# Performance work log

Measured on AMD Instinct MI355X. Metric: run time of the kernel, lower is better.

## Reference

```python
import jax, jax.numpy as jnp
import numpy as np

EPS = 1e-10
R, H, W = 8192, 1024, 1024


def setup_inputs() -> dict:
    key = jax.random.key(0)
    k1, k2, k3, k4, k5, k6 = jax.random.split(key, 6)
    seg = jax.random.normal(k1, (1, 2, H, W), dtype=jnp.float32)
    score = jax.random.uniform(k2, (R, 1), dtype=jnp.float32)
    # boxes with guaranteed non-empty regions (x2>x1, y2>y1)
    x1 = jax.random.randint(k3, (R,), 0, W - 1)
    y1 = jax.random.randint(k4, (R,), 0, H - 1)
    w = jax.random.randint(k5, (R,), 1, W)
    h = jax.random.randint(k6, (R,), 1, H)
    x2 = jnp.minimum(x1 + w, W)
    y2 = jnp.minimum(y1 + h, H)
    ssw = jnp.stack([jnp.zeros_like(x1), x1, y1, x2, y2], axis=1)[None].astype(jnp.int32)
    return {"ssw": ssw, "seg": seg, "score": score}


def reference(ssw, seg, score):
    boxes = ssw[0, :, 1:]                      # [R,4] = x1,y1,x2,y2
    seg = jax.nn.softmax(seg, axis=1)
    score_map = seg[0, 1]                      # [H,W]
    # Summed-area table: region mean for every ROI in one vectorized pass
    # (replaces the per-ROI python-loop slicing in the original).
    P = jnp.pad(jnp.cumsum(jnp.cumsum(score_map, axis=0), axis=1), ((1, 0), (1, 0)))
    x1, y1, x2, y2 = boxes[:, 0], boxes[:, 1], boxes[:, 2], boxes[:, 3]
    sums = P[y2, x2] - P[y1, x2] - P[y2, x1] + P[y1, x1]
    area = ((y2 - y1) * (x2 - x1)).astype(score_map.dtype)
    iou = sums / area                          # [R] per-ROI mean score
    # pairwise smooth-abs differences
    sim_iou = jnp.sqrt((iou[:, None] - iou[None, :]) ** 2 + EPS)     # [R,R]
    s = score.reshape(-1)
    sim_score = jnp.sqrt((s[:, None] - s[None, :]) ** 2 + EPS)        # [R,R]
    return jnp.mean((sim_iou - sim_score) ** 2)
```

## Files before the change

### kernel.cpp

```cpp
#include <hip/hip_runtime.h>
#include <math.h>

#define HH 1024
#define WW 1024
#define RR 8192
#define EPSD 1e-10

#define OFF_C     4194304
#define OFF_BSUM  12582912
#define OFF_IOU   13107200
#define OFF_STAT  13139968

__device__ __forceinline__ float sigm(float a, float b) {
    float z = (a - b) * 1.44269504088896f;
    float e = __builtin_amdgcn_exp2f(z);
    return __builtin_amdgcn_rcpf(1.0f + e);
}

__global__ void row_scan(const float* __restrict__ seg, float* __restrict__ rowpref,
                         double* __restrict__ stats) {
    if (blockIdx.x == 0 && threadIdx.x < 5) stats[threadIdx.x] = 0.0;
    const int h = blockIdx.x;
    const int t = threadIdx.x;
    const float4* s0 = (const float4*)(seg + (size_t)h * WW);
    const float4* s1 = (const float4*)(seg + (size_t)(HH * WW) + (size_t)h * WW);
    float4 a = s0[t];
    float4 b = s1[t];
    float p0 = sigm(a.x, b.x);
    float p1 = p0 + sigm(a.y, b.y);
    float p2 = p1 + sigm(a.z, b.z);
    float p3 = p2 + sigm(a.w, b.w);

    float tsum = p3;
    const int lane = t & 63, wid = t >> 6;
    #pragma unroll
    for (int off = 1; off < 64; off <<= 1) {
        float n = __shfl_up(tsum, off, 64);
        if (lane >= off) tsum += n;
    }
    __shared__ float wsum[4];
    if (lane == 63) wsum[wid] = tsum;
    __syncthreads();
    float woff = 0.0f;
    for (int k = 0; k < wid; ++k) woff += wsum[k];
    const float excl = woff + tsum - p3;

    float4 o;
    o.x = excl + p0;
    o.y = excl + p1;
    o.z = excl + p2;
    o.w = excl + p3;
    ((float4*)(rowpref + (size_t)h * WW))[t] = o;
}

__global__ void col_partial(const float* __restrict__ rowpref, double* __restrict__ bsum) {
    const int w = blockIdx.x * 256 + threadIdx.x;
    const int chunk = blockIdx.y;
    const int r0 = chunk * 16;
    double acc = 0.0;
    #pragma unroll
    for (int r = r0; r < r0 + 16; ++r) acc += (double)rowpref[(size_t)r * WW + w];
    bsum[chunk * WW + w] = acc;
}

__global__ void col_scan(const float* __restrict__ rowpref, const double* __restrict__ bsum,
                         double* __restrict__ C) {
    const int w = blockIdx.x * 256 + threadIdx.x;
    const int chunk = blockIdx.y;
    double acc = 0.0;
    for (int k = 0; k < chunk; ++k) acc += bsum[k * WW + w];
    const int r0 = chunk * 16;
    #pragma unroll
    for (int r = r0; r < r0 + 16; ++r) {
        acc += (double)rowpref[(size_t)r * WW + w];
        C[(size_t)r * WW + w] = acc;
    }
}

__global__ void box_stats(const int* __restrict__ ssw, const double* __restrict__ C,
                          const float* __restrict__ score,
                          float* __restrict__ iou, double* __restrict__ stats) {
    const int r = blockIdx.x * 256 + threadIdx.x;
    const int* b = ssw + r * 5;
    const int x1 = b[1], y1 = b[2], x2 = b[3], y2 = b[4];
    double p22 = C[(size_t)(y2 - 1) * WW + (x2 - 1)];
    double p12 = (y1 > 0) ? C[(size_t)(y1 - 1) * WW + (x2 - 1)] : 0.0;
    double p21 = (x1 > 0) ? C[(size_t)(y2 - 1) * WW + (x1 - 1)] : 0.0;
    double p11 = (y1 > 0 && x1 > 0) ? C[(size_t)(y1 - 1) * WW + (x1 - 1)] : 0.0;
    double sums = p22 - p12 - p21 + p11;
    double area = (double)((y2 - y1) * (x2 - x1));
    double u = sums / area;
    iou[r] = (float)u;
    double s = (double)score[r];

    double v0 = u, v1 = u * u, v2 = s, v3 = s * s;
    #pragma unroll
    for (int off = 32; off; off >>= 1) {
        v0 += __shfl_down(v0, off, 64);
        v1 += __shfl_down(v1, off, 64);
        v2 += __shfl_down(v2, off, 64);
        v3 += __shfl_down(v3, off, 64);
    }
    if ((threadIdx.x & 63) == 0) {
        atomicAdd(&stats[0], v0);
        atomicAdd(&stats[1], v1);
        atomicAdd(&stats[2], v2);
        atomicAdd(&stats[3], v3);
    }
}

#define KI 4
#define JT 128
__global__ void pair_prod(const float* __restrict__ iou, const float* __restrict__ score,
                          double* __restrict__ stats) {
    __shared__ float ju[JT];
    __shared__ float js[JT];
    const int t = threadIdx.x;
    const int j0 = blockIdx.y * JT;
    if (t < JT) ju[t] = iou[j0 + t];
    else js[t - JT] = score[j0 + t - JT];

    const int i0 = blockIdx.x * (256 * KI) + t;
    float iu[KI], isc[KI];
    #pragma unroll
    for (int k = 0; k < KI; ++k) {
        iu[k]  = iou[i0 + 256 * k];
        isc[k] = score[i0 + 256 * k];
    }
    __syncthreads();

    float acc[KI];
    #pragma unroll
    for (int k = 0; k < KI; ++k) acc[k] = 0.0f;
    #pragma unroll 8
    for (int j = 0; j < JT; ++j) {
        const float uj = ju[j];
        const float sj = js[j];
        #pragma unroll
        for (int k = 0; k < KI; ++k) {
            float du = iu[k] - uj;
            float ds = isc[k] - sj;
            acc[k] += fabsf(du * ds);
        }
    }
    float afl = (acc[0] + acc[1]) + (acc[2] + acc[3]);
    double v = (double)afl;
    #pragma unroll
    for (int off = 32; off; off >>= 1) v += __shfl_down(v, off, 64);
    __shared__ double wred[4];
    const int lane = t & 63, wid = t >> 6;
    if (lane == 0) wred[wid] = v;
    __syncthreads();
    if (t == 0) atomicAdd(&stats[4], wred[0] + wred[1] + wred[2] + wred[3]);
}

__global__ void finalize(const double* __restrict__ stats, float* __restrict__ out) {
    const double R = (double)RR;
    double Su = stats[0], Su2 = stats[1], Ss = stats[2], Ss2 = stats[3], Sab = stats[4];
    double lossR2 = 2.0 * R * Su2 - 2.0 * Su * Su
                  + 2.0 * R * Ss2 - 2.0 * Ss * Ss
                  + 2.0 * R * R * EPSD
                  - 2.0 * Sab;
    out[0] = (float)(lossR2 / (R * R));
}

extern "C" void kernel_launch(void* const* d_in, const int* in_sizes, int n_in,
                              void* d_out, int out_size, void* d_ws, size_t ws_size,
                              hipStream_t stream) {
    const int*   ssw   = (const int*)d_in[0];
    const float* seg   = (const float*)d_in[1];
    const float* score = (const float*)d_in[2];

    float*  rowpref = (float*)d_ws;
    double* C       = (double*)((char*)d_ws + OFF_C);
    double* bsum    = (double*)((char*)d_ws + OFF_BSUM);
    float*  iou     = (float*)((char*)d_ws + OFF_IOU);
    double* stats   = (double*)((char*)d_ws + OFF_STAT);

    row_scan<<<HH, 256, 0, stream>>>(seg, rowpref, stats);
    col_partial<<<dim3(4, 64), 256, 0, stream>>>(rowpref, bsum);
    col_scan<<<dim3(4, 64), 256, 0, stream>>>(rowpref, bsum, C);
    box_stats<<<RR / 256, 256, 0, stream>>>(ssw, C, score, iou, stats);
    pair_prod<<<dim3(RR / (256 * KI), RR / JT), 256, 0, stream>>>(iou, score, stats);
    finalize<<<1, 1, 0, stream>>>(stats, (float*)d_out);
}
```

Before: 108.4 us.

## Fuse column scan passes via flag chaining and fold finalize into pair kernel

```diff
diff --git a/kernel.cpp b/kernel.cpp
--- a/kernel.cpp
+++ b/kernel.cpp
@@ -10,6 +10,10 @@
 #define OFF_BSUM  12582912
 #define OFF_IOU   13107200
 #define OFF_STAT  13139968
+#define OFF_FLAG  13140032
+#define OFF_TICK  13141056
+
+typedef float v2f __attribute__((ext_vector_type(2)));
 
 __device__ __forceinline__ float sigm(float a, float b) {
     float z = (a - b) * 1.44269504088896f;
@@ -17,9 +21,16 @@
     return __builtin_amdgcn_rcpf(1.0f + e);
 }
 
-__global__ void row_scan(const float* __restrict__ seg, float* __restrict__ rowpref,
-                         double* __restrict__ stats) {
-    if (blockIdx.x == 0 && threadIdx.x < 5) stats[threadIdx.x] = 0.0;
+__global__ __launch_bounds__(256) void row_scan(const float* __restrict__ seg,
+                                                float* __restrict__ rowpref,
+                                                double* __restrict__ stats,
+                                                unsigned* __restrict__ flags,
+                                                unsigned* __restrict__ ticket) {
+    if (blockIdx.x == 0) {
+        if (threadIdx.x < 5) stats[threadIdx.x] = 0.0;
+        flags[threadIdx.x] = 0u;
+        if (threadIdx.x == 0) *ticket = 0u;
+    }
     const int h = blockIdx.x;
     const int t = threadIdx.x;
     const float4* s0 = (const float4*)(seg + (size_t)h * WW);
@@ -53,34 +64,53 @@
     ((float4*)(rowpref + (size_t)h * WW))[t] = o;
 }
 
-__global__ void col_partial(const float* __restrict__ rowpref, double* __restrict__ bsum) {
-    const int w = blockIdx.x * 256 + threadIdx.x;
+__global__ __launch_bounds__(256) void col_scan_fused(const float* __restrict__ rowpref,
+                                                      double* __restrict__ bsum,
+                                                      double* __restrict__ C,
+                                                      unsigned* __restrict__ flags) {
+    const int c = blockIdx.x;
     const int chunk = blockIdx.y;
+    const int t = threadIdx.x;
+    const int w = c * 256 + t;
     const int r0 = chunk * 16;
+
+    double part[16];
     double acc = 0.0;
     #pragma unroll
-    for (int r = r0; r < r0 + 16; ++r) acc += (double)rowpref[(size_t)r * WW + w];
+    for (int r = 0; r < 16; ++r) {
+        acc += (double)rowpref[(size_t)(r0 + r) * WW + w];
+        part[r] = acc;
+    }
     bsum[chunk * WW + w] = acc;
-}
-
-__global__ void col_scan(const float* __restrict__ rowpref, const double* __restrict__ bsum,
-                         double* __restrict__ C) {
-    const int w = blockIdx.x * 256 + threadIdx.x;
-    const int chunk = blockIdx.y;
-    double acc = 0.0;
-    for (int k = 0; k < chunk; ++k) acc += bsum[k * WW + w];
-    const int r0 = chunk * 16;
-    #pragma unroll
-    for (int r = r0; r < r0 + 16; ++r) {
-        acc += (double)rowpref[(size_t)r * WW + w];
-        C[(size_t)r * WW + w] = acc;
-    }
-}
-
-__global__ void box_stats(const int* __restrict__ ssw, const double* __restrict__ C,
-                          const float* __restrict__ score,
-                          float* __restrict__ iou, double* __restrict__ stats) {
-    const int r = blockIdx.x * 256 + threadIdx.x;
+    __syncthreads();
+    __threadfence();
+    if (t == 0)
+        __hip_atomic_store(&flags[chunk * 4 + c], 1u,
+                           __ATOMIC_RELEASE, __HIP_MEMORY_SCOPE_AGENT);
+
+    if (t == 0) {
+        for (int kp = 0; kp < chunk; ++kp)
+            while (__hip_atomic_load(&flags[kp * 4 + c],
+                                     __ATOMIC_RELAXED, __HIP_MEMORY_SCOPE_AGENT) == 0u) {}
+    }
+    __syncthreads();
+    __threadfence();
+
+    double base = 0.0;
+    #pragma unroll 4
+    for (int kp = 0; kp < chunk; ++kp) base += bsum[kp * WW + w];
+
+    #pragma unroll
+    for (int r = 0; r < 16; ++r)
+        C[(size_t)(r0 + r) * WW + w] = base + part[r];
+}
+
+__global__ __launch_bounds__(128) void box_stats(const int* __restrict__ ssw,
+                                                 const double* __restrict__ C,
+                                                 const float* __restrict__ score,
+                                                 float* __restrict__ iou,
+                                                 double* __restrict__ stats) {
+    const int r = blockIdx.x * 128 + threadIdx.x;
     const int* b = ssw + r * 5;
     const int x1 = b[1], y1 = b[2], x2 = b[3], y2 = b[4];
     double p22 = C[(size_t)(y2 - 1) * WW + (x2 - 1)];
@@ -111,39 +141,47 @@
 
 #define KI 4
 #define JT 128
-__global__ void pair_prod(const float* __restrict__ iou, const float* __restrict__ score,
-                          double* __restrict__ stats) {
-    __shared__ float ju[JT];
-    __shared__ float js[JT];
+__global__ __launch_bounds__(256) void pair_prod(const float* __restrict__ iou,
+                                                 const float* __restrict__ score,
+                                                 double* __restrict__ stats,
+                                                 float* __restrict__ out,
+                                                 unsigned* __restrict__ ticket) {
+    __shared__ v2f ju[JT / 2];
+    __shared__ v2f js[JT / 2];
     const int t = threadIdx.x;
     const int j0 = blockIdx.y * JT;
-    if (t < JT) ju[t] = iou[j0 + t];
-    else js[t - JT] = score[j0 + t - JT];
+    if (t < JT / 2) ju[t] = ((const v2f*)(iou + j0))[t];
+    else if (t < JT) js[t - JT / 2] = ((const v2f*)(score + j0))[t - JT / 2];
 
     const int i0 = blockIdx.x * (256 * KI) + t;
-    float iu[KI], isc[KI];
+    v2f iuv[KI], isv[KI];
     #pragma unroll
     for (int k = 0; k < KI; ++k) {
-        iu[k]  = iou[i0 + 256 * k];
-        isc[k] = score[i0 + 256 * k];
-    }
-    __syncthreads();
-
-    float acc[KI];
-    #pragma unroll
-    for (int k = 0; k < KI; ++k) acc[k] = 0.0f;
-    #pragma unroll 8
-    for (int j = 0; j < JT; ++j) {
-        const float uj = ju[j];
-        const float sj = js[j];
+        float u = iou[i0 + 256 * k];
+        float s = score[i0 + 256 * k];
+        iuv[k] = (v2f){u, u};
+        isv[k] = (v2f){s, s};
+    }
+    __syncthreads();
+
+    float ax[KI], ay[KI];
+    #pragma unroll
+    for (int k = 0; k < KI; ++k) { ax[k] = 0.0f; ay[k] = 0.0f; }
+    #pragma unroll 4
+    for (int j = 0; j < JT / 2; ++j) {
+        const v2f uj = ju[j];
+        const v2f sj = js[j];
         #pragma unroll
         for (int k = 0; k < KI; ++k) {
-            float du = iu[k] - uj;
-            float ds = isc[k] - sj;
-            acc[k] += fabsf(du * ds);
+            v2f du = iuv[k] - uj;
+            v2f ds = isv[k] - sj;
+            v2f p  = du * ds;
+            ax[k] += fabsf(p.x);
+            ay[k] += fabsf(p.y);
         }
     }
-    float afl = (acc[0] + acc[1]) + (acc[2] + acc[3]);
+    float afl = ((ax[0] + ay[0]) + (ax[1] + ay[1]))
+              + ((ax[2] + ay[2]) + (ax[3] + ay[3]));
     double v = (double)afl;
     #pragma unroll
     for (int off = 32; off; off >>= 1) v += __shfl_down(v, off, 64);
@@ -151,17 +189,25 @@
     const int lane = t & 63, wid = t >> 6;
     if (lane == 0) wred[wid] = v;
     __syncthreads();
-    if (t == 0) atomicAdd(&stats[4], wred[0] + wred[1] + wred[2] + wred[3]);
-}
-
-__global__ void finalize(const double* __restrict__ stats, float* __restrict__ out) {
-    const double R = (double)RR;
-    double Su = stats[0], Su2 = stats[1], Ss = stats[2], Ss2 = stats[3], Sab = stats[4];
-    double lossR2 = 2.0 * R * Su2 - 2.0 * Su * Su
-                  + 2.0 * R * Ss2 - 2.0 * Ss * Ss
-                  + 2.0 * R * R * EPSD
-                  - 2.0 * Sab;
-    out[0] = (float)(lossR2 / (R * R));
+    if (t == 0) {
+        atomicAdd(&stats[4], wred[0] + wred[1] + wred[2] + wred[3]);
+        __threadfence();
+        unsigned tk = atomicAdd(ticket, 1u);
+        if (tk == (unsigned)(gridDim.x * gridDim.y - 1)) {
+            __threadfence();
+            double Su  = __hip_atomic_load(&stats[0], __ATOMIC_RELAXED, __HIP_MEMORY_SCOPE_AGENT);
+            double Su2 = __hip_atomic_load(&stats[1], __ATOMIC_RELAXED, __HIP_MEMORY_SCOPE_AGENT);
+            double Ss  = __hip_atomic_load(&stats[2], __ATOMIC_RELAXED, __HIP_MEMORY_SCOPE_AGENT);
+            double Ss2 = __hip_atomic_load(&stats[3], __ATOMIC_RELAXED, __HIP_MEMORY_SCOPE_AGENT);
+            double Sab = __hip_atomic_load(&stats[4], __ATOMIC_RELAXED, __HIP_MEMORY_SCOPE_AGENT);
+            const double R = (double)RR;
+            double lossR2 = 2.0 * R * Su2 - 2.0 * Su * Su
+                          + 2.0 * R * Ss2 - 2.0 * Ss * Ss
+                          + 2.0 * R * R * EPSD
+                          - 2.0 * Sab;
+            out[0] = (float)(lossR2 / (R * R));
+        }
+    }
 }
 
 extern "C" void kernel_launch(void* const* d_in, const int* in_sizes, int n_in,
@@ -171,16 +217,16 @@
     const float* seg   = (const float*)d_in[1];
     const float* score = (const float*)d_in[2];
 
-    float*  rowpref = (float*)d_ws;
-    double* C       = (double*)((char*)d_ws + OFF_C);
-    double* bsum    = (double*)((char*)d_ws + OFF_BSUM);
-    float*  iou     = (float*)((char*)d_ws + OFF_IOU);
-    double* stats   = (double*)((char*)d_ws + OFF_STAT);
-
-    row_scan<<<HH, 256, 0, stream>>>(seg, rowpref, stats);
-    col_partial<<<dim3(4, 64), 256, 0, stream>>>(rowpref, bsum);
-    col_scan<<<dim3(4, 64), 256, 0, stream>>>(rowpref, bsum, C);
-    box_stats<<<RR / 256, 256, 0, stream>>>(ssw, C, score, iou, stats);
-    pair_prod<<<dim3(RR / (256 * KI), RR / JT), 256, 0, stream>>>(iou, score, stats);
-    finalize<<<1, 1, 0, stream>>>(stats, (float*)d_out);
-}
+    float*    rowpref = (float*)d_ws;
+    double*   C       = (double*)((char*)d_ws + OFF_C);
+    double*   bsum    = (double*)((char*)d_ws + OFF_BSUM);
+    float*    iou     = (float*)((char*)d_ws + OFF_IOU);
+    double*   stats   = (double*)((char*)d_ws + OFF_STAT);
+    unsigned* flags   = (unsigned*)((char*)d_ws + OFF_FLAG);
+    unsigned* ticket  = (unsigned*)((char*)d_ws + OFF_TICK);
+
+    row_scan<<<HH, 256, 0, stream>>>(seg, rowpref, stats, flags, ticket);
+    col_scan_fused<<<dim3(4, 64), 256, 0, stream>>>(rowpref, bsum, C, flags);
+    box_stats<<<RR / 128, 128, 0, stream>>>(ssw, C, score, iou, stats);
+    pair_prod<<<dim3(RR / (256 * KI), RR / JT), 256, 0, stream>>>(iou, score, stats, (float*)d_out, ticket);
+}
```

Result: slower. 143.7 us (+32.6%).
